# Kernel optimization log

Hardware: AMD Instinct MI355X
Metric: run time of the kernel (lower is better)

The kernel has to match this reference:

```python
import jax, jax.numpy as jnp
import numpy as np

N = 100000        # nodes
E = 1600000       # edges (avg degree 16)
D = 128           # feature dim (in_dim == out_dim)
L = 3             # num_layers
P = 8             # num_parts


def setup_inputs() -> dict:
    key = jax.random.key(0)
    k1, k2, k3, k4, k5, k6 = jax.random.split(key, 6)
    edge_row = jnp.sort(jax.random.randint(k1, (E,), 0, N))
    edge_col = jax.random.randint(k2, (E,), 0, N)
    edge_vals = jax.random.uniform(k3, (E,), dtype=jnp.float32)
    x = jax.random.normal(k4, (N, D), dtype=jnp.float32)
    stacked_params = jax.random.normal(k5, (L, D, D, P), dtype=jnp.float32)
    layer_weights = jax.random.normal(k6, (L, P), dtype=jnp.float32)
    return {"edge_row": edge_row, "edge_col": edge_col, "edge_vals": edge_vals,
            "x": x, "stacked_params": stacked_params, "layer_weights": layer_weights}


def reference(edge_row, edge_col, edge_vals, x, stacked_params, layer_weights):
    n = x.shape[0]
    num_layers = stacked_params.shape[0]
    h = x
    for i in range(num_layers):
        # sparse adj.spmm(h): gather source features, scale by edge value, sum per row
        msg = h[edge_col] * edge_vals[:, None]                       # [E, D]
        ax = jax.ops.segment_sum(msg, edge_row, num_segments=n)      # [N, D]
        # MyLinear: softmax over the num_parts weight, contract parts dim
        w = jax.nn.softmax(layer_weights[i])                         # [P]
        ww = jnp.einsum('oip,p->oi', stacked_params[i], w)           # [D_out, D_in]
        h = ax @ ww.T                                                # [N, D_out]
        if i < num_layers - 1:
            h = jax.nn.relu(h)
    return h
```

## Files before the change

### kernel.cpp

```cpp
#include <hip/hip_runtime.h>
#include <cstdint>

#define D 128
#define P 8
#define L 3

typedef __attribute__((ext_vector_type(8))) _Float16 f16x8;
typedef __attribute__((ext_vector_type(4))) float    f32x4;
typedef __attribute__((ext_vector_type(2))) float    f32x2;

#if __has_builtin(__builtin_amdgcn_cvt_pk_f32_fp8) && __has_builtin(__builtin_amdgcn_cvt_pk_fp8_f32)
#define HAVE_FP8_CVT 1
#else
#define HAVE_FP8_CVT 0
#endif

template<bool HI>
static __device__ __forceinline__ f32x2 fp8_pair(uint32_t u) {
#if HAVE_FP8_CVT
    return __builtin_amdgcn_cvt_pk_f32_fp8((int)u, HI);
#else
    uint32_t w = HI ? (u >> 16) : u;
    f32x2 r;
#pragma unroll
    for (int i = 0; i < 2; i++) {
        uint32_t b = (w >> (8 * i)) & 0xffu;
        uint32_t mag = b & 0x7fu;
        uint16_t h = (uint16_t)(((b & 0x80u) << 8) | ((mag >= 8u) ? ((mag << 7) + 0x2000u) : 0u));
        union { uint16_t q; _Float16 hf; } c; c.q = h;
        r[i] = (float)c.hf;
    }
    return r;
#endif
}

static __device__ __forceinline__ uint32_t f32_to_fp8(float v) {
#if HAVE_FP8_CVT
    return (uint32_t)__builtin_amdgcn_cvt_pk_fp8_f32(v, v, 0, false) & 0xffu;
#else
    union { _Float16 hf; uint16_t q; } c; c.hf = (_Float16)v;
    uint32_t s = ((uint32_t)c.q >> 8) & 0x80u;
    int t = (int)(c.q & 0x7fff) - 0x2000;
    if (t < 0) return s;
    int r = (t + 63 + ((t >> 7) & 1)) >> 7;
    if (r > 0x7e) r = 0x7e;
    return s | (uint32_t)r;
#endif
}

__global__ void prep_edges(const int* __restrict__ er, const int* __restrict__ col,
                           const float* __restrict__ vals,
                           int* __restrict__ rp, uint32_t* __restrict__ epk,
                           int n, int e) {
    int i = blockIdx.x * blockDim.x + threadIdx.x;
    if (i >= e) return;
    union { _Float16 h; uint16_t u; } v;
    v.h = (_Float16)vals[i];
    epk[i] = ((uint32_t)col[i] << 15) | (uint32_t)(v.u & 0x7FFFu);

    int cur = er[i];
    if (i == 0) {
        for (int r = 0; r <= cur; r++) rp[r] = 0;
    } else {
        int prev = er[i - 1];
        for (int r = prev + 1; r <= cur; r++) rp[r] = i;
    }
    if (i == e - 1) {
        for (int r = cur + 1; r <= n; r++) rp[r] = e;
    }
}

__global__ void build_ww(const float* __restrict__ sp, const float* __restrict__ lw,
                         _Float16* __restrict__ wwB) {
    int idx = blockIdx.x * blockDim.x + threadIdx.x;
    if (idx >= L * D * D) return;
    int l = idx / (D * D);
    int rem = idx - l * D * D;
    int o = rem / D;
    int i = rem - o * D;
    float wv[P];
    float m = -1e30f;
#pragma unroll
    for (int p = 0; p < P; p++) { wv[p] = lw[l * P + p]; m = fmaxf(m, wv[p]); }
    float s = 0.f;
#pragma unroll
    for (int p = 0; p < P; p++) { wv[p] = __expf(wv[p] - m); s += wv[p]; }
    float inv = 1.0f / s;
    const float* spp = sp + ((size_t)(l * D + o) * D + i) * P;
    float acc = 0.f;
#pragma unroll
    for (int p = 0; p < P; p++) acc += spp[p] * wv[p];
    int kt = i >> 5, kp = i & 31;
    wwB[(((l * 4 + kt) * D + o) << 5) + kp] = (_Float16)(acc * inv);
}

static __device__ __forceinline__ void mfma_store32_q8(const _Float16 (*s_h)[136],
                                                       const _Float16* __restrict__ wwB_l,
                                                       uint8_t* __restrict__ y8,
                                                       float* __restrict__ scl,
                                                       unsigned* srow,
                                                       int row0, int n, int tid) {
    const int w = tid >> 6, lane = tid & 63;
    const int quad = lane >> 4, l16 = lane & 15;
    f32x4 acc[2][2] = {};
#pragma unroll
    for (int kt = 0; kt < 4; kt++) {
        f16x8 af0 = *(const f16x8*)&s_h[l16][kt * 32 + quad * 8];
        f16x8 af1 = *(const f16x8*)&s_h[16 + l16][kt * 32 + quad * 8];
#pragma unroll
        for (int c = 0; c < 2; c++) {
            const int ct = w * 2 + c;
            f16x8 bf = *(const f16x8*)&wwB_l[((kt * D + ct * 16 + l16) << 5) + quad * 8];
            acc[0][c] = __builtin_amdgcn_mfma_f32_16x16x32_f16(af0, bf, acc[0][c], 0, 0, 0);
            acc[1][c] = __builtin_amdgcn_mfma_f32_16x16x32_f16(af1, bf, acc[1][c], 0, 0, 0);
        }
    }
#pragma unroll
    for (int rt = 0; rt < 2; rt++) {
#pragma unroll
        for (int rg = 0; rg < 4; rg++) {
            float m = fmaxf(fabsf(acc[rt][0][rg]), fabsf(acc[rt][1][rg]));
#pragma unroll
            for (int d = 1; d < 16; d <<= 1) m = fmaxf(m, __shfl_xor(m, d));
            if (l16 == 0) atomicMax(&srow[rt * 16 + quad * 4 + rg], __float_as_uint(m));
        }
    }
    __syncthreads();
#pragma unroll
    for (int rt = 0; rt < 2; rt++) {
#pragma unroll
        for (int rg = 0; rg < 4; rg++) {
            const int rr = rt * 16 + quad * 4 + rg;
            const int row = row0 + rr;
            float rmax = fmaxf(__uint_as_float(srow[rr]), 1e-20f);
            float qs = 448.f / rmax;
            if (row < n) {
#pragma unroll
                for (int c = 0; c < 2; c++) {
                    const int ct = w * 2 + c;
                    float v = acc[rt][c][rg] * qs;
                    v = fminf(fmaxf(v, -448.f), 448.f);
                    y8[row * D + ct * 16 + l16] = (uint8_t)f32_to_fp8(v);
                }
                if (w == 0 && l16 == 0) scl[row] = rmax * (1.f / 448.f);
            }
        }
    }
}

__global__ __launch_bounds__(256, 8)
void gemm_x32(const float* __restrict__ x, const _Float16* __restrict__ wwB_l,
              uint8_t* __restrict__ y8, float* __restrict__ scl, int n) {
    __shared__ _Float16 s_h[32][136];
    __shared__ unsigned srow[32];
    const int tid = threadIdx.x;
    const int row0 = blockIdx.x * 32;
    const int c8 = (tid & 15) * 8;
    if (tid < 32) srow[tid] = 0;
    {
        int r = tid >> 4;
#pragma unroll
        for (int h2 = 0; h2 < 2; h2++) {
            int rr = r + h2 * 16;
            int row = row0 + rr;
            float4 v0 = {}, v1 = {};
            if (row < n) {
                v0 = *(const float4*)&x[row * D + c8];
                v1 = *(const float4*)&x[row * D + c8 + 4];
            }
            f16x8 h;
            h[0] = (_Float16)v0.x; h[1] = (_Float16)v0.y;
            h[2] = (_Float16)v0.z; h[3] = (_Float16)v0.w;
            h[4] = (_Float16)v1.x; h[5] = (_Float16)v1.y;
            h[6] = (_Float16)v1.z; h[7] = (_Float16)v1.w;
            *(f16x8*)&s_h[rr][c8] = h;
        }
    }
    __syncthreads();
    mfma_store32_q8(s_h, wwB_l, y8, scl, srow, row0, n, tid);
}

template<int NB>
static __device__ __forceinline__ void gather_chunk16(float (&a)[16],
                                                      const uint8_t* __restrict__ y8,
                                                      const uint32_t* __restrict__ epk,
                                                      const float* __restrict__ scl,
                                                      int e, int c16) {
    uint32_t m[NB];
#pragma unroll
    for (int j = 0; j < NB; j++) m[j] = epk[e + j];
    uint4 g[NB]; float sc[NB];
#pragma unroll
    for (int j = 0; j < NB; j++) {
        uint32_t row = m[j] >> 15;
        g[j]  = *(const uint4*)&y8[row * (uint32_t)D + (uint32_t)c16];
        sc[j] = scl[row];
    }
#pragma unroll
    for (int j = 0; j < NB; j++) {
        union { uint16_t u; _Float16 h; } vv; vv.u = (uint16_t)(m[j] & 0x7FFFu);
        float vf = (float)vv.h * sc[j];
        f32x2 p;
        p = fp8_pair<false>(g[j].x); a[ 0] += vf * p[0]; a[ 1] += vf * p[1];
        p = fp8_pair<true >(g[j].x); a[ 2] += vf * p[0]; a[ 3] += vf * p[1];
        p = fp8_pair<false>(g[j].y); a[ 4] += vf * p[0]; a[ 5] += vf * p[1];
        p = fp8_pair<true >(g[j].y); a[ 6] += vf * p[0]; a[ 7] += vf * p[1];
        p = fp8_pair<false>(g[j].z); a[ 8] += vf * p[0]; a[ 9] += vf * p[1];
        p = fp8_pair<true >(g[j].z); a[10] += vf * p[0]; a[11] += vf * p[1];
        p = fp8_pair<false>(g[j].w); a[12] += vf * p[0]; a[13] += vf * p[1];
        p = fp8_pair<true >(g[j].w); a[14] += vf * p[0]; a[15] += vf * p[1];
    }
}

static __device__ __forceinline__ void gather_row16(float (&a)[16],
                                                    const uint8_t* __restrict__ y8,
                                                    const uint32_t* __restrict__ epk,
                                                    const float* __restrict__ scl,
                                                    int e, int e1, int c16) {
    for (; e + 4 <= e1; e += 4) gather_chunk16<4>(a, y8, epk, scl, e, c16);
    for (; e < e1; e++) gather_chunk16<1>(a, y8, epk, scl, e, c16);
}

__global__ __launch_bounds__(256, 8)
void fused_layer(const uint8_t* __restrict__ yprev, const float* __restrict__ sprev,
                 const int* __restrict__ rp, const uint32_t* __restrict__ epk,
                 const _Float16* __restrict__ wwB_l,
                 uint8_t* __restrict__ ynext, float* __restrict__ snext, int n) {
    __shared__ _Float16 s_h[32][136];
    __shared__ unsigned srow[32];
    const int tid = threadIdx.x;
    const int row0 = blockIdx.x * 32;
    const int sg = tid >> 3;
    const int c16 = (tid & 7) * 16;
    if (tid < 32) srow[tid] = 0;
    {
        int r = row0 + sg;
        float a[16] = {};
        if (r < n) gather_row16(a, yprev, epk, sprev, rp[r], rp[r + 1], c16);
        f16x8 o0, o1;
#pragma unroll
        for (int k = 0; k < 8; k++) {
            o0[k] = (_Float16)fmaxf(a[k], 0.f);
            o1[k] = (_Float16)fmaxf(a[8 + k], 0.f);
        }
        *(f16x8*)&s_h[sg][c16]     = o0;
        *(f16x8*)&s_h[sg][c16 + 8] = o1;
    }
    __syncthreads();
    mfma_store32_q8(s_h, wwB_l, ynext, snext, srow, row0, n, tid);
}

__global__ __launch_bounds__(256, 8)
void spmm_f32(const uint8_t* __restrict__ y8, const float* __restrict__ sprev,
              const int* __restrict__ rp, const uint32_t* __restrict__ epk,
              float* __restrict__ out, int n) {
    const int tid = threadIdx.x;
    const int r = blockIdx.x * 32 + (tid >> 3);
    const int c16 = (tid & 7) * 16;
    if (r >= n) return;
    float a[16] = {};
    gather_row16(a, y8, epk, sprev, rp[r], rp[r + 1], c16);
    float* o = &out[(size_t)r * D + c16];
    *(float4*)&o[ 0] = make_float4(a[ 0], a[ 1], a[ 2], a[ 3]);
    *(float4*)&o[ 4] = make_float4(a[ 4], a[ 5], a[ 6], a[ 7]);
    *(float4*)&o[ 8] = make_float4(a[ 8], a[ 9], a[10], a[11]);
    *(float4*)&o[12] = make_float4(a[12], a[13], a[14], a[15]);
}

extern "C" void kernel_launch(void* const* d_in, const int* in_sizes, int n_in,
                              void* d_out, int out_size, void* d_ws, size_t ws_size,
                              hipStream_t stream) {
    const int*   edge_row  = (const int*)d_in[0];
    const int*   edge_col  = (const int*)d_in[1];
    const float* edge_vals = (const float*)d_in[2];
    const float* x         = (const float*)d_in[3];
    const float* sp        = (const float*)d_in[4];
    const float* lw        = (const float*)d_in[5];
    float* out = (float*)d_out;

    const int E_ = in_sizes[0];
    const int N_ = in_sizes[3] / D;

    char* ws = (char*)d_ws;
    int* row_ptr = (int*)ws;
    size_t off = (((size_t)(N_ + 1) * sizeof(int)) + 255) & ~(size_t)255;
    uint32_t* epk = (uint32_t*)(ws + off);
    off += (size_t)E_ * sizeof(uint32_t);
    off = (off + 255) & ~(size_t)255;
    _Float16* wwB = (_Float16*)(ws + off);
    off += (size_t)L * 4 * D * 32 * sizeof(_Float16);
    off = (off + 255) & ~(size_t)255;
    uint8_t* y8A = (uint8_t*)(ws + off);
    off += (size_t)N_ * D;
    uint8_t* y8B = (uint8_t*)(ws + off);
    off += (size_t)N_ * D;
    off = (off + 255) & ~(size_t)255;
    float* scA = (float*)(ws + off);
    off += (size_t)N_ * sizeof(float);
    float* scB = (float*)(ws + off);

    prep_edges<<<(E_ + 255) / 256, 256, 0, stream>>>(edge_row, edge_col, edge_vals,
                                                     row_ptr, epk, N_, E_);
    build_ww<<<(L * D * D + 255) / 256, 256, 0, stream>>>(sp, lw, wwB);

    const int sblk = (N_ + 31) / 32;
    const int WWL = 4 * D * 32;

    gemm_x32<<<sblk, 256, 0, stream>>>(x, wwB, y8A, scA, N_);
    fused_layer<<<sblk, 256, 0, stream>>>(y8A, scA, row_ptr, epk, wwB + WWL,     y8B, scB, N_);
    fused_layer<<<sblk, 256, 0, stream>>>(y8B, scB, row_ptr, epk, wwB + 2 * WWL, y8A, scA, N_);
    spmm_f32<<<sblk, 256, 0, stream>>>(y8A, scA, row_ptr, epk, out, N_);
}
```

Before: 283.8 us.

## Stage gathered neighbor rows into LDS via async global_load_lds triple buffering

Replaces the per-thread register gather in the SpMM with a per-wave pipeline. Each wave stages edge metadata into LDS, then issues global_load_lds copies of the 32-edge chunks of fp8 neighbor rows and their scales into a triple buffer. Threads accumulate from LDS using an XOR-swizzled layout. Occupancy hints drop from 8 to 2 waves per EU, a trade of latency hiding from many waves for explicit prefetch. The LDS footprint grows substantially, and the hand-written vmcnt waits must match the number of loads issued per chunk.

```diff
diff --git a/kernel.cpp b/kernel.cpp
--- a/kernel.cpp
+++ b/kernel.cpp
@@ -4,6 +4,10 @@
 #define D 128
 #define P 8
 #define L 3
+
+#define CHUNK 32
+#define NBUF 3
+#define MAXE 256
 
 typedef __attribute__((ext_vector_type(8))) _Float16 f16x8;
 typedef __attribute__((ext_vector_type(4))) float    f32x4;
@@ -14,6 +18,21 @@
 #else
 #define HAVE_FP8_CVT 0
 #endif
+
+typedef const __attribute__((address_space(1))) void* gas_t;
+typedef __attribute__((address_space(3))) void*       las_t;
+static __device__ __forceinline__ void glds16(const void* g, void* l) {
+    __builtin_amdgcn_global_load_lds((gas_t)g, (las_t)l, 16, 0, 0);
+}
+static __device__ __forceinline__ void glds4(const void* g, void* l) {
+    __builtin_amdgcn_global_load_lds((gas_t)g, (las_t)l, 4, 0, 0);
+}
+static __device__ __forceinline__ void waitvm0() {
+    asm volatile("s_waitcnt vmcnt(0)" ::: "memory");
+}
+static __device__ __forceinline__ void waitvm5() {
+    asm volatile("s_waitcnt vmcnt(5)" ::: "memory");
+}
 
 template<bool HI>
 static __device__ __forceinline__ f32x2 fp8_pair(uint32_t u) {
@@ -57,7 +76,6 @@
     union { _Float16 h; uint16_t u; } v;
     v.h = (_Float16)vals[i];
     epk[i] = ((uint32_t)col[i] << 15) | (uint32_t)(v.u & 0x7FFFu);
-
     int cur = er[i];
     if (i == 0) {
         for (int r = 0; r <= cur; r++) rp[r] = 0;
@@ -180,63 +198,100 @@
     mfma_store32_q8(s_h, wwB_l, y8, scl, srow, row0, n, tid);
 }
 
-template<int NB>
-static __device__ __forceinline__ void gather_chunk16(float (&a)[16],
-                                                      const uint8_t* __restrict__ y8,
-                                                      const uint32_t* __restrict__ epk,
-                                                      const float* __restrict__ scl,
-                                                      int e, int c16) {
-    uint32_t m[NB];
-#pragma unroll
-    for (int j = 0; j < NB; j++) m[j] = epk[e + j];
-    uint4 g[NB]; float sc[NB];
-#pragma unroll
-    for (int j = 0; j < NB; j++) {
-        uint32_t row = m[j] >> 15;
-        g[j]  = *(const uint4*)&y8[row * (uint32_t)D + (uint32_t)c16];
-        sc[j] = scl[row];
-    }
-#pragma unroll
-    for (int j = 0; j < NB; j++) {
-        union { uint16_t u; _Float16 h; } vv; vv.u = (uint16_t)(m[j] & 0x7FFFu);
-        float vf = (float)vv.h * sc[j];
-        f32x2 p;
-        p = fp8_pair<false>(g[j].x); a[ 0] += vf * p[0]; a[ 1] += vf * p[1];
-        p = fp8_pair<true >(g[j].x); a[ 2] += vf * p[0]; a[ 3] += vf * p[1];
-        p = fp8_pair<false>(g[j].y); a[ 4] += vf * p[0]; a[ 5] += vf * p[1];
-        p = fp8_pair<true >(g[j].y); a[ 6] += vf * p[0]; a[ 7] += vf * p[1];
-        p = fp8_pair<false>(g[j].z); a[ 8] += vf * p[0]; a[ 9] += vf * p[1];
-        p = fp8_pair<true >(g[j].z); a[10] += vf * p[0]; a[11] += vf * p[1];
-        p = fp8_pair<false>(g[j].w); a[12] += vf * p[0]; a[13] += vf * p[1];
-        p = fp8_pair<true >(g[j].w); a[14] += vf * p[0]; a[15] += vf * p[1];
-    }
-}
-
-static __device__ __forceinline__ void gather_row16(float (&a)[16],
-                                                    const uint8_t* __restrict__ y8,
-                                                    const uint32_t* __restrict__ epk,
-                                                    const float* __restrict__ scl,
-                                                    int e, int e1, int c16) {
-    for (; e + 4 <= e1; e += 4) gather_chunk16<4>(a, y8, epk, scl, e, c16);
-    for (; e < e1; e++) gather_chunk16<1>(a, y8, epk, scl, e, c16);
-}
-
-__global__ __launch_bounds__(256, 8)
+static __device__ __forceinline__ void gather_rows_staged(
+        float (&a)[16],
+        const uint8_t* __restrict__ y8, const float* __restrict__ scl,
+        const int* __restrict__ rp, const uint32_t* __restrict__ epk,
+        uint8_t (*s_stage)[CHUNK * 128], float (*s_sclb)[CHUNK * 2],
+        uint32_t* s_epk, int row0w, int n, int lane) {
+    const int sgid = lane >> 3;
+    const int l8 = lane & 7;
+    const int r = row0w + sgid;
+    int e0r = 0, e1r = 0;
+    if (r < n) { e0r = rp[r]; e1r = rp[r + 1]; }
+    const int rlo = row0w < n ? row0w : n;
+    int rhi = row0w + 8; rhi = rhi < n ? rhi : n;
+    const int e0w = rp[rlo];
+    const int e1w = rp[rhi < rlo ? rlo : rhi];
+
+    for (int wb = e0w; wb < e1w; wb += MAXE) {
+        const int wcnt = (e1w - wb) < MAXE ? (e1w - wb) : MAXE;
+        const int nch = (wcnt + CHUNK - 1) / CHUNK;
+        glds16(epk + wb + lane * 4, s_epk);
+        waitvm0();
+
+        auto stage_chunk = [&](int cc) {
+            const int bi = cc % NBUF;
+            const int erel0 = cc * CHUNK;
+#pragma unroll
+            for (int k = 0; k < 4; k++) {
+                int er = erel0 + k * 8 + sgid;
+                er = er < wcnt ? er : wcnt - 1;
+                uint32_t m = s_epk[er];
+                const uint8_t* gp = y8 + (size_t)(m >> 15) * D + ((l8 ^ sgid) << 4);
+                glds16(gp, (void*)&s_stage[bi][k * 1024]);
+            }
+            {
+                int er = erel0 + (lane >> 1);
+                er = er < wcnt ? er : wcnt - 1;
+                uint32_t m = s_epk[er];
+                glds4(scl + (m >> 15), (void*)&s_sclb[bi][0]);
+            }
+        };
+
+        stage_chunk(0);
+        stage_chunk(1);
+        for (int c = 0; c < nch; c++) {
+            waitvm5();
+            const int bi = c % NBUF;
+            const int cb = wb + c * CHUNK;
+            int s0 = e0r > cb ? e0r : cb;
+            int t0 = e1r < cb + CHUNK ? e1r : cb + CHUNK;
+            for (int e = s0; e < t0; e++) {
+                const int slot = e - cb;
+                const int sw = (l8 ^ (slot & 7)) << 4;
+                uint4 g = *(const uint4*)&s_stage[bi][slot * 128 + sw];
+                uint32_t mv = s_epk[e - wb];
+                union { uint16_t u; _Float16 h; } vv; vv.u = (uint16_t)(mv & 0x7FFFu);
+                float coef = s_sclb[bi][slot * 2] * (float)vv.h;
+                f32x2 p;
+                p = fp8_pair<false>(g.x); a[ 0] += coef * p[0]; a[ 1] += coef * p[1];
+                p = fp8_pair<true >(g.x); a[ 2] += coef * p[0]; a[ 3] += coef * p[1];
+                p = fp8_pair<false>(g.y); a[ 4] += coef * p[0]; a[ 5] += coef * p[1];
+                p = fp8_pair<true >(g.y); a[ 6] += coef * p[0]; a[ 7] += coef * p[1];
+                p = fp8_pair<false>(g.z); a[ 8] += coef * p[0]; a[ 9] += coef * p[1];
+                p = fp8_pair<true >(g.z); a[10] += coef * p[0]; a[11] += coef * p[1];
+                p = fp8_pair<false>(g.w); a[12] += coef * p[0]; a[13] += coef * p[1];
+                p = fp8_pair<true >(g.w); a[14] += coef * p[0]; a[15] += coef * p[1];
+            }
+            stage_chunk(c + 2);
+        }
+    }
+}
+
+__global__ __launch_bounds__(256)
+__attribute__((amdgpu_waves_per_eu(2, 2)))
 void fused_layer(const uint8_t* __restrict__ yprev, const float* __restrict__ sprev,
                  const int* __restrict__ rp, const uint32_t* __restrict__ epk,
                  const _Float16* __restrict__ wwB_l,
                  uint8_t* __restrict__ ynext, float* __restrict__ snext, int n) {
+    __shared__ __align__(16) uint8_t  s_stage[4][NBUF][CHUNK * 128];
+    __shared__ __align__(16) float    s_sclb [4][NBUF][CHUNK * 2];
+    __shared__ __align__(16) uint32_t s_epk  [4][MAXE];
     __shared__ _Float16 s_h[32][136];
     __shared__ unsigned srow[32];
     const int tid = threadIdx.x;
+    const int lane = tid & 63;
+    const int w = tid >> 6;
     const int row0 = blockIdx.x * 32;
-    const int sg = tid >> 3;
-    const int c16 = (tid & 7) * 16;
     if (tid < 32) srow[tid] = 0;
+
+    float a[16] = {};
+    gather_rows_staged(a, yprev, sprev, rp, epk,
+                       s_stage[w], s_sclb[w], s_epk[w], row0 + w * 8, n, lane);
     {
-        int r = row0 + sg;
-        float a[16] = {};
-        if (r < n) gather_row16(a, yprev, epk, sprev, rp[r], rp[r + 1], c16);
+        const int sg = tid >> 3;
+        const int c16 = (lane & 7) * 16;
         f16x8 o0, o1;
 #pragma unroll
         for (int k = 0; k < 8; k++) {
@@ -250,17 +305,25 @@
     mfma_store32_q8(s_h, wwB_l, ynext, snext, srow, row0, n, tid);
 }
 
-__global__ __launch_bounds__(256, 8)
+__global__ __launch_bounds__(256)
+__attribute__((amdgpu_waves_per_eu(2, 2)))
 void spmm_f32(const uint8_t* __restrict__ y8, const float* __restrict__ sprev,
               const int* __restrict__ rp, const uint32_t* __restrict__ epk,
               float* __restrict__ out, int n) {
+    __shared__ __align__(16) uint8_t  s_stage[4][NBUF][CHUNK * 128];
+    __shared__ __align__(16) float    s_sclb [4][NBUF][CHUNK * 2];
+    __shared__ __align__(16) uint32_t s_epk  [4][MAXE];
     const int tid = threadIdx.x;
-    const int r = blockIdx.x * 32 + (tid >> 3);
-    const int c16 = (tid & 7) * 16;
+    const int lane = tid & 63;
+    const int w = tid >> 6;
+    const int row0 = blockIdx.x * 32;
+
+    float a[16] = {};
+    gather_rows_staged(a, y8, sprev, rp, epk,
+                       s_stage[w], s_sclb[w], s_epk[w], row0 + w * 8, n, lane);
+    const int r = row0 + (tid >> 3);
     if (r >= n) return;
-    float a[16] = {};
-    gather_row16(a, y8, epk, sprev, rp[r], rp[r + 1], c16);
-    float* o = &out[(size_t)r * D + c16];
+    float* o = &out[(size_t)r * D + (lane & 7) * 16];
     *(float4*)&o[ 0] = make_float4(a[ 0], a[ 1], a[ 2], a[ 3]);
     *(float4*)&o[ 4] = make_float4(a[ 4], a[ 5], a[ 6], a[ 7]);
     *(float4*)&o[ 8] = make_float4(a[ 8], a[ 9], a[10], a[11]);
```

Result: slower. 447.5 us (+57.7%).
